# Kernel tuning notes

Hardware: AMD Instinct MI355X
Metric: run time of the kernel (lower is better)

Reference implementation:

```python
import jax, jax.numpy as jnp
import numpy as np
import math

B, L = 4, 2048
D_MODEL, N_HEADS, D_K, D_V, D_FF, FACTOR = 512, 8, 64, 64, 2048, 5


def _layernorm(x, g, b, eps=1e-5):
    m = x.mean(-1, keepdims=True)
    v = jnp.mean((x - m) ** 2, axis=-1, keepdims=True)
    return (x - m) * jax.lax.rsqrt(v + eps) * g + b


def setup_inputs() -> dict:
    key = jax.random.key(0)
    ks = jax.random.split(key, 8)
    w = lambda k, shape: (jax.random.normal(k, shape, jnp.float32) * 0.02)
    sample_k = min(FACTOR * int(math.ceil(math.log(L))), L)  # c*ln(L_K) sampled keys per query
    return {
        "x": jax.random.normal(ks[0], (B, L, D_MODEL), jnp.float32),
        "Wq": w(ks[1], (D_MODEL, N_HEADS * D_K)),
        "Wk": w(ks[2], (D_MODEL, N_HEADS * D_K)),
        "Wv": w(ks[3], (D_MODEL, N_HEADS * D_V)),
        "Wo": w(ks[4], (N_HEADS * D_V, D_MODEL)),
        "ln1_g": jnp.ones((D_MODEL,), jnp.float32),
        "ln1_b": jnp.zeros((D_MODEL,), jnp.float32),
        "conv1_w": w(ks[5], (D_FF, D_MODEL)),
        "conv1_b": jnp.zeros((D_FF,), jnp.float32),
        "conv2_w": w(ks[6], (D_MODEL, D_FF)),
        "conv2_b": jnp.zeros((D_MODEL,), jnp.float32),
        "ln2_g": jnp.ones((D_MODEL,), jnp.float32),
        "ln2_b": jnp.zeros((D_MODEL,), jnp.float32),
        # Informer samples sample_k random keys per query position (constant indices)
        "sample_idx": jax.random.randint(ks[7], (L, sample_k), 0, L),
    }


def reference(x, Wq, Wk, Wv, Wo, ln1_g, ln1_b, conv1_w, conv1_b, conv2_w, conv2_b, ln2_g, ln2_b, sample_idx):
    Bx, Lx, D = x.shape
    H = N_HEADS
    # projections -> [B,H,L,d]
    Q = (x @ Wq).reshape(Bx, Lx, H, D_K).transpose(0, 2, 1, 3)
    K = (x @ Wk).reshape(Bx, Lx, H, D_K).transpose(0, 2, 1, 3)
    V = (x @ Wv).reshape(Bx, Lx, H, D_V).transpose(0, 2, 1, 3)

    u = min(FACTOR * int(math.ceil(math.log(Lx))), Lx)  # top-u active queries
    # sampled QK scores: [B,H,L,sample_k]
    K_samp = K[:, :, sample_idx]                              # [B,H,L,S,dk]
    qk_s = jnp.einsum('bhle,bhlse->bhls', Q, K_samp)
    # sparsity measure M = max - mean (Informer divides sum by L_K)
    M = qk_s.max(-1) - qk_s.sum(-1) / Lx                      # [B,H,L]
    _, top = jax.lax.top_k(M, u)                              # [B,H,u]

    Q_red = jnp.take_along_axis(Q, top[..., None], axis=2)    # [B,H,u,dk]
    scores = jnp.einsum('bhue,bhle->bhul', Q_red, K) / math.sqrt(D_K)
    attn = jax.nn.softmax(scores, axis=-1)                    # [B,H,u,L]

    # initial context = mean of V over keys; update only top-u query rows
    ctx = jnp.broadcast_to(V.mean(axis=2, keepdims=True), V.shape)  # [B,H,L,dv]
    upd = jnp.einsum('bhul,bhld->bhud', attn, V)              # [B,H,u,dv]
    bi = jnp.arange(Bx)[:, None, None]
    hi = jnp.arange(H)[None, :, None]
    ctx = ctx.at[bi, hi, top].set(upd)

    out = ctx.transpose(0, 2, 1, 3).reshape(Bx, Lx, H * D_V) @ Wo
    x1 = _layernorm(x + out, ln1_g, ln1_b)  # residual + norm inside attention sublayer

    # conv1d(k=1) FFN == per-token linear; dropout is identity in eval
    y = jax.nn.gelu(x1 @ conv1_w.T + conv1_b, approximate=False)
    y = y @ conv2_w.T + conv2_b
    return _layernorm(x1 + y, ln2_g, ln2_b)
```

## Files before the change

### kernel.cpp

```cpp
#include <hip/hip_runtime.h>
#include <hip/hip_bf16.h>

#define BB 4
#define LL 2048
#define DD 512
#define HH 8
#define DKK 64
#define FF 2048

typedef __bf16  bf16x8  __attribute__((ext_vector_type(8)));
typedef float   floatx4 __attribute__((ext_vector_type(4)));

__device__ __forceinline__ void async_cp16(const void* g, void* l) {
    __builtin_amdgcn_global_load_lds(
        (const __attribute__((address_space(1))) unsigned int*)g,
        (__attribute__((address_space(3))) unsigned int*)l,
        16, 0, 0);
}

__global__ __launch_bounds__(256) void prep_w(
    const float* __restrict__ Wq, const float* __restrict__ Wk,
    const float* __restrict__ Wv, const float* __restrict__ Wo,
    __bf16* __restrict__ wb)
{
    const size_t SZ = (size_t)DD * DD;
    int z = blockIdx.z;
    const float* s = (z == 0) ? Wq : (z == 1) ? Wk : (z == 2) ? Wv : Wo;
    __bf16* hi; __bf16* lo = nullptr;
    if (z == 0)      { hi = wb;          lo = wb + SZ; }
    else if (z == 1) { hi = wb + 2 * SZ; lo = wb + 3 * SZ; }
    else if (z == 2) { hi = wb + 4 * SZ; }
    else             { hi = wb + 5 * SZ; }
    int idx = blockIdx.x * 256 + threadIdx.x;
    int k = idx >> 9, n = idx & 511;
    float v = s[idx];
    __bf16 h = (__bf16)v;
    hi[(size_t)n * DD + k] = h;
    if (lo) lo[(size_t)n * DD + k] = (__bf16)(v - (float)h);
}

__global__ __launch_bounds__(256) void cast_cw(
    const float* __restrict__ c1w, const float* __restrict__ c2w,
    __bf16* __restrict__ d1, __bf16* __restrict__ d2)
{
    const float* s = blockIdx.z ? c2w : c1w;
    __bf16* d = blockIdx.z ? d2 : d1;
    int idx = blockIdx.x * 256 + threadIdx.x;
    d[idx] = (__bf16)s[idx];
}

__global__ __launch_bounds__(256) void split_cast_x(
    const float* __restrict__ x, __bf16* __restrict__ xhi, __bf16* __restrict__ xlo)
{
    int idx = blockIdx.x * 256 + threadIdx.x;
    float v = x[idx];
    __bf16 h = (__bf16)v;
    xhi[idx] = h;
    xlo[idx] = (__bf16)(v - (float)h);
}

template<int ACT, bool BIAS, bool OUT_BF16>
__global__ __launch_bounds__(256) void gemm_mfma(
    const __bf16* __restrict__ A, const __bf16* __restrict__ B,
    const float* __restrict__ bias, void* __restrict__ Cv,
    int M, int N, int K)
{
    __shared__ __bf16 As[2][128 * 32];
    __shared__ __bf16 Bs[2][128 * 32];
    const int tid = threadIdx.x;
    const int wave = tid >> 6, lane = tid & 63;
    const int gx = gridDim.x;
    const int nwg = gx * gridDim.y;
    const int hw = blockIdx.y * gx + blockIdx.x;
    const int virt = ((nwg & 7) == 0) ? ((hw & 7) * (nwg >> 3) + (hw >> 3)) : hw;
    const int m0 = (virt / gx) * 128, n0 = (virt % gx) * 128;
    const int wm = (wave >> 1) * 64, wn = (wave & 1) * 64;
    const int l15 = lane & 15, kq = lane >> 4;

    auto stage = [&](int buf, int k0) {
        #pragma unroll
        for (int p = 0; p < 2; p++) {
            int c = p * 256 + tid;
            int row = c >> 2, col = (c & 3) * 8;
            async_cp16(A + (size_t)(m0 + row) * K + k0 + col, &As[buf][c * 8]);
            async_cp16(B + (size_t)(n0 + row) * K + k0 + col, &Bs[buf][c * 8]);
        }
    };

    floatx4 acc[4][4] = {};

    stage(0, 0);
    __syncthreads();
    int cur = 0;
    for (int k0 = 0; k0 < K; k0 += 32) {
        if (k0 + 32 < K) stage(cur ^ 1, k0 + 32);
        bf16x8 af[4], bfr[4];
        #pragma unroll
        for (int i = 0; i < 4; i++)
            af[i] = *(const bf16x8*)(&As[cur][(wm + i * 16 + l15) * 32 + kq * 8]);
        #pragma unroll
        for (int j = 0; j < 4; j++)
            bfr[j] = *(const bf16x8*)(&Bs[cur][(wn + j * 16 + l15) * 32 + kq * 8]);
        #pragma unroll
        for (int i = 0; i < 4; i++)
            #pragma unroll
            for (int j = 0; j < 4; j++)
                acc[i][j] = __builtin_amdgcn_mfma_f32_16x16x32_bf16(af[i], bfr[j], acc[i][j], 0, 0, 0);
        __syncthreads();
        cur ^= 1;
    }
    #pragma unroll
    for (int i = 0; i < 4; i++) {
        #pragma unroll
        for (int j = 0; j < 4; j++) {
            int col = n0 + wn + j * 16 + l15;
            float bv = BIAS ? bias[col] : 0.0f;
            #pragma unroll
            for (int r = 0; r < 4; r++) {
                int row = m0 + wm + i * 16 + kq * 4 + r;
                float v = acc[i][j][r] + bv;
                if (ACT == 1) v = 0.5f * v * (1.0f + erff(v * 0.70710678118654752f));
                if (OUT_BF16) ((__bf16*)Cv)[(size_t)row * N + col] = (__bf16)v;
                else          ((float*)Cv)[(size_t)row * N + col] = v;
            }
        }
    }
}

__global__ __launch_bounds__(256) void gemm_mfma_split(
    const __bf16* __restrict__ Ah, const __bf16* __restrict__ Al,
    const __bf16* __restrict__ Bh, const __bf16* __restrict__ Bl,
    float* __restrict__ C, int M, int N, int K)
{
    __shared__ __bf16 Ahs[2][128 * 32];
    __shared__ __bf16 Als[2][128 * 32];
    __shared__ __bf16 Bhs[2][128 * 32];
    __shared__ __bf16 Bls[2][128 * 32];
    const int tid = threadIdx.x;
    const int wave = tid >> 6, lane = tid & 63;
    const int gx = gridDim.x;
    const int nwg = gx * gridDim.y;
    const int hw = blockIdx.y * gx + blockIdx.x;
    const int virt = ((nwg & 7) == 0) ? ((hw & 7) * (nwg >> 3) + (hw >> 3)) : hw;
    const int m0 = (virt / gx) * 128, n0 = (virt % gx) * 128;
    const int wm = (wave >> 1) * 64, wn = (wave & 1) * 64;
    const int l15 = lane & 15, kq = lane >> 4;

    auto stage = [&](int buf, int k0) {
        #pragma unroll
        for (int p = 0; p < 2; p++) {
            int c = p * 256 + tid;
            int row = c >> 2, col = (c & 3) * 8;
            size_t goA = (size_t)(m0 + row) * K + k0 + col;
            size_t goB = (size_t)(n0 + row) * K + k0 + col;
            async_cp16(Ah + goA, &Ahs[buf][c * 8]);
            async_cp16(Al + goA, &Als[buf][c * 8]);
            async_cp16(Bh + goB, &Bhs[buf][c * 8]);
            async_cp16(Bl + goB, &Bls[buf][c * 8]);
        }
    };

    floatx4 acc[4][4] = {};

    stage(0, 0);
    __syncthreads();
    int cur = 0;
    for (int k0 = 0; k0 < K; k0 += 32) {
        if (k0 + 32 < K) stage(cur ^ 1, k0 + 32);
        bf16x8 ah[4], al[4], bh[4], bl[4];
        #pragma unroll
        for (int i = 0; i < 4; i++) {
            int off = (wm + i * 16 + l15) * 32 + kq * 8;
            ah[i] = *(const bf16x8*)(&Ahs[cur][off]);
            al[i] = *(const bf16x8*)(&Als[cur][off]);
        }
        #pragma unroll
        for (int j = 0; j < 4; j++) {
            int off = (wn + j * 16 + l15) * 32 + kq * 8;
            bh[j] = *(const bf16x8*)(&Bhs[cur][off]);
            bl[j] = *(const bf16x8*)(&Bls[cur][off]);
        }
        #pragma unroll
        for (int i = 0; i < 4; i++)
            #pragma unroll
            for (int j = 0; j < 4; j++) {
                acc[i][j] = __builtin_amdgcn_mfma_f32_16x16x32_bf16(ah[i], bh[j], acc[i][j], 0, 0, 0);
                acc[i][j] = __builtin_amdgcn_mfma_f32_16x16x32_bf16(ah[i], bl[j], acc[i][j], 0, 0, 0);
                acc[i][j] = __builtin_amdgcn_mfma_f32_16x16x32_bf16(al[i], bh[j], acc[i][j], 0, 0, 0);
            }
        __syncthreads();
        cur ^= 1;
    }
    #pragma unroll
    for (int i = 0; i < 4; i++)
        #pragma unroll
        for (int j = 0; j < 4; j++) {
            int col = n0 + wn + j * 16 + l15;
            #pragma unroll
            for (int r = 0; r < 4; r++) {
                int row = m0 + wm + i * 16 + kq * 4 + r;
                C[(size_t)row * N + col] = acc[i][j][r];
            }
        }
}

__device__ __forceinline__ float dpp_sum16(float p) {
    int t;
    t = __builtin_amdgcn_update_dpp(0, __float_as_int(p), 0xB1,  0xF, 0xF, true);
    p += __int_as_float(t);
    t = __builtin_amdgcn_update_dpp(0, __float_as_int(p), 0x4E,  0xF, 0xF, true);
    p += __int_as_float(t);
    t = __builtin_amdgcn_update_dpp(0, __float_as_int(p), 0x141, 0xF, 0xF, true);
    p += __int_as_float(t);
    t = __builtin_amdgcn_update_dpp(0, __float_as_int(p), 0x140, 0xF, 0xF, true);
    p += __int_as_float(t);
    return p;
}

__global__ __launch_bounds__(256) void calc_m(
    const float* __restrict__ Q, const float* __restrict__ Kb,
    const int* __restrict__ sidx, float* __restrict__ Mo, int U)
{
    __shared__ int   js[64];
    __shared__ float red_mx[2][HH];
    __shared__ float red_sm[2][HH];
    int i = blockIdx.x;
    int b = i & 3, l = i >> 2;
    int tid = threadIdx.x;
    if (tid < U) js[tid] = sidx[l * U + tid];
    int e    = (tid & 127) * 4;
    int slot = tid >> 7;
    const float* qr = Q + ((size_t)(b * LL + l) * DD);
    float4 q = *(const float4*)(qr + e);
    const float* kbase = Kb + ((size_t)b * LL) * DD + e;
    __syncthreads();
    float mx = -1e30f, sm = 0.f;
    for (int s = slot; s < U; s += 2) {
        int j = js[s];
        float4 kv = *(const float4*)(kbase + (size_t)j * DD);
        float p = q.x * kv.x + q.y * kv.y + q.z * kv.z + q.w * kv.w;
        p = dpp_sum16(p);
        mx = fmaxf(mx, p);
        sm += p;
    }
    if ((tid & 15) == 0) {
        int head = (tid >> 4) & 7;
        red_mx[slot][head] = mx;
        red_sm[slot][head] = sm;
    }
    __syncthreads();
    if (tid < HH) {
        float m2 = fmaxf(red_mx[0][tid], red_mx[1][tid]);
        float s2 = red_sm[0][tid] + red_sm[1][tid];
        Mo[((size_t)(b * HH + tid)) * LL + l] = m2 - s2 * (1.0f / (float)LL);
    }
}

__global__ __launch_bounds__(256) void topk_k(
    const float* __restrict__ Mo, int* __restrict__ top, int U)
{
    __shared__ unsigned int hist[256];
    __shared__ unsigned int wsum[4];
    __shared__ unsigned int bc[2];
    __shared__ int ties[LL];
    __shared__ int cnt2[2];
    int bh = blockIdx.x, tid = threadIdx.x;
    int lane = tid & 63, w = tid >> 6;

    unsigned int my[8];
    #pragma unroll
    for (int i = 0; i < 8; i++) {
        unsigned int u = __float_as_uint(Mo[(size_t)bh * LL + tid + i * 256]);
        my[i] = u ^ ((u >> 31) ? 0xFFFFFFFFu : 0x80000000u);
    }

    unsigned int prefix = 0, pmask = 0;
    unsigned int need = (unsigned int)U;
    unsigned int above = 0;

    for (int pass = 0; pass < 4; pass++) {
        int shift = 24 - pass * 8;
        hist[tid] = 0;
        __syncthreads();
        #pragma unroll
        for (int i = 0; i < 8; i++) {
            unsigned int u = my[i];
            if ((u & pmask) == prefix)
                atomicAdd(&hist[(u >> shift) & 255u], 1u);
        }
        __syncthreads();
        unsigned int h = hist[tid];
        #pragma unroll
        for (int off = 1; off < 64; off <<= 1) {
            unsigned int o = __shfl_down(h, off);
            if (lane + off < 64) h += o;
        }
        if (lane == 0) wsum[w] = h;
        __syncthreads();
        unsigned int tail = 0;
        #pragma unroll
        for (int w2 = 1; w2 < 4; w2++) if (w2 > w) tail += wsum[w2];
        h += tail;
        hist[tid] = h;
        __syncthreads();
        unsigned int St = h;
        unsigned int St1 = (tid < 255) ? hist[tid + 1] : 0u;
        if (St >= need && St1 < need) { bc[0] = (unsigned int)tid; bc[1] = St1; }
        __syncthreads();
        unsigned int dig = bc[0], abv = bc[1];
        above += abv;
        need -= abv;
        prefix |= dig << shift;
        pmask |= 0xFFu << shift;
        __syncthreads();
    }

    if (tid == 0) { cnt2[0] = 0; cnt2[1] = 0; }
    __syncthreads();
    #pragma unroll
    for (int i = 0; i < 8; i++) {
        unsigned int u = my[i];
        int idx = tid + i * 256;
        if (u > prefix) {
            int pos = atomicAdd(&cnt2[0], 1);
            top[bh * U + pos] = idx;
        } else if (u == prefix) {
            int pos = atomicAdd(&cnt2[1], 1);
            ties[pos] = idx;
        }
    }
    __syncthreads();
    int tcnt = cnt2[1];
    #pragma unroll
    for (int i = 0; i < 8; i++) {
        unsigned int u = my[i];
        if (u == prefix) {
            int idx = tid + i * 256;
            int rank = 0;
            for (int j = 0; j < tcnt; j++) rank += (ties[j] < idx) ? 1 : 0;
            if (rank < (int)need) top[bh * U + (int)above + rank] = idx;
        }
    }
}

__global__ __launch_bounds__(256) void vmean_k(
    const __bf16* __restrict__ V, float* __restrict__ Vm)
{
    __shared__ float osum[4][DKK];
    int bh = blockIdx.x;
    int b = bh >> 3, h = bh & 7;
    int tid = threadIdx.x, d = tid & 63, part = tid >> 6;
    const __bf16* vp = V + ((size_t)(b * LL + part * 512) * DD + h * DKK + d);
    float s = 0.f;
    for (int i = 0; i < 512; i++) s += (float)vp[(size_t)i * DD];
    osum[part][d] = s;
    __syncthreads();
    if (tid < DKK)
        Vm[bh * DKK + tid] = (osum[0][tid] + osum[1][tid] + osum[2][tid] + osum[3][tid]) * (1.0f / (float)LL);
}

__global__ __launch_bounds__(256) void gather_qred(
    const float* __restrict__ Q, const int* __restrict__ top,
    __bf16* __restrict__ qred, int U)
{
    int bh = blockIdx.y;
    int b = bh >> 3, h = bh & 7;
    int e = blockIdx.x * 256 + threadIdx.x;
    int u = e >> 6, d = e & 63;
    float v = 0.f;
    if (u < U) {
        int l = top[bh * U + u];
        v = Q[((size_t)(b * LL + l) * DD + h * DKK) + d] * 0.125f;
    }
    qred[(size_t)bh * 48 * DKK + e] = (__bf16)v;
}

__global__ __launch_bounds__(256) void gemm_s(
    const __bf16* __restrict__ qred, const float* __restrict__ Kb,
    float* __restrict__ S)
{
    __shared__ __bf16 Qs[2 * 48 * 32];
    __shared__ __bf16 Ks[2 * 128 * 32];
    int bh = blockIdx.y, nc = blockIdx.x;
    int b = bh >> 3, h = bh & 7, l0 = nc * 128;
    int tid = threadIdx.x;
    const unsigned int* qsrc = (const unsigned int*)(qred + (size_t)bh * 48 * DKK);
    unsigned int* qdst = (unsigned int*)Qs;
    #pragma unroll
    for (int t = 0; t < 6; t++) {
        int ui = tid + t * 256;
        int u = ui >> 5, kp = ui & 31;
        int p = kp >> 4, kl2 = kp & 15;
        qdst[p * 768 + u * 16 + kl2] = qsrc[ui];
    }
    #pragma unroll
    for (int t = 0; t < 8; t++) {
        int fi = tid + t * 256;
        int row = fi >> 4, k4 = fi & 15;
        int p = k4 >> 3, kl = (k4 & 7) * 4;
        float4 kv = *(const float4*)(Kb + ((size_t)(b * LL + l0 + row) * DD + h * DKK + k4 * 4));
        __bf16* dst = Ks + p * 128 * 32 + row * 32 + kl;
        dst[0] = (__bf16)kv.x; dst[1] = (__bf16)kv.y;
        dst[2] = (__bf16)kv.z; dst[3] = (__bf16)kv.w;
    }
    __syncthreads();
    int wave = tid >> 6, lane = tid & 63, l15 = lane & 15, kq = lane >> 4;
    floatx4 acc[3][2] = {};
    #pragma unroll
    for (int p = 0; p < 2; p++) {
        bf16x8 bq[2];
        #pragma unroll
        for (int j = 0; j < 2; j++)
            bq[j] = *(const bf16x8*)(Ks + p * 4096 + (wave * 32 + j * 16 + l15) * 32 + kq * 8);
        #pragma unroll
        for (int i = 0; i < 3; i++) {
            bf16x8 aq = *(const bf16x8*)(Qs + p * 1536 + (i * 16 + l15) * 32 + kq * 8);
            #pragma unroll
            for (int j = 0; j < 2; j++)
                acc[i][j] = __builtin_amdgcn_mfma_f32_16x16x32_bf16(aq, bq[j], acc[i][j], 0, 0, 0);
        }
    }
    #pragma unroll
    for (int i = 0; i < 3; i++)
        #pragma unroll
        for (int j = 0; j < 2; j++) {
            int col = l0 + wave * 32 + j * 16 + l15;
            #pragma unroll
            for (int r = 0; r < 4; r++) {
                int row = i * 16 + kq * 4 + r;
                S[((size_t)bh * 48 + row) * LL + col] = acc[i][j][r];
            }
        }
}

__global__ __launch_bounds__(256) void softmax_p(float* __restrict__ S, int U)
{
    __shared__ float red[256];
    int row = blockIdx.x;
    int bh = row / U, u = row % U;
    float* sr = S + ((size_t)bh * 48 + u) * LL;
    int tid = threadIdx.x;
    float sc[8]; float mx = -1e30f;
    #pragma unroll
    for (int i = 0; i < 8; i++) { sc[i] = sr[tid + i * 256]; mx = fmaxf(mx, sc[i]); }
    red[tid] = mx; __syncthreads();
    for (int s = 128; s > 0; s >>= 1) { if (tid < s) red[tid] = fmaxf(red[tid], red[tid + s]); __syncthreads(); }
    mx = red[0]; __syncthreads();
    float se = 0.f;
    #pragma unroll
    for (int i = 0; i < 8; i++) { sc[i] = __expf(sc[i] - mx); se += sc[i]; }
    red[tid] = se; __syncthreads();
    for (int s = 128; s > 0; s >>= 1) { if (tid < s) red[tid] += red[tid + s]; __syncthreads(); }
    float inv = 1.0f / red[0];
    __bf16* pr = (__bf16*)sr;
    #pragma unroll
    for (int i = 0; i < 8; i++) pr[tid + i * 256] = (__bf16)(sc[i] * inv);
}

__global__ __launch_bounds__(256) void pv_k(
    const float* __restrict__ S, const __bf16* __restrict__ V,
    float* __restrict__ upd, int U)
{
    __shared__ __bf16 pls[4 * LL];
    __shared__ float osum[4][4][DKK];
    int bh = blockIdx.y, uc = blockIdx.x;
    int b = bh >> 3, h = bh & 7, tid = threadIdx.x;
    #pragma unroll
    for (int t = 0; t < 16; t++) {
        int ui = tid + t * 256;
        int up = ui >> 10, lw = ui & 1023;
        const unsigned int* src = (const unsigned int*)(S + ((size_t)bh * 48 + uc * 4 + up) * LL);
        ((unsigned int*)pls)[up * 1024 + lw] = src[lw];
    }
    __syncthreads();
    int d = tid & 63, part = tid >> 6;
    float a0 = 0.f, a1 = 0.f, a2 = 0.f, a3 = 0.f;
    const __bf16* vp = V + ((size_t)(b * LL + part * 512) * DD + h * DKK + d);
    int lbase = part * 512;
    for (int i = 0; i < 512; i++) {
        float v = (float)vp[(size_t)i * DD];
        int l = lbase + i;
        a0 += (float)pls[l] * v;
        a1 += (float)pls[LL + l] * v;
        a2 += (float)pls[2 * LL + l] * v;
        a3 += (float)pls[3 * LL + l] * v;
    }
    osum[part][0][d] = a0; osum[part][1][d] = a1;
    osum[part][2][d] = a2; osum[part][3][d] = a3;
    __syncthreads();
    int u2 = tid >> 6;
    float s = osum[0][u2][d] + osum[1][u2][d] + osum[2][u2][d] + osum[3][u2][d];
    upd[((size_t)bh * U + uc * 4 + u2) * DKK + d] = s;
}

__global__ __launch_bounds__(256) void ctx_init(
    const float* __restrict__ Vm, __bf16* __restrict__ ctx)
{
    int idx = blockIdx.x * 256 + threadIdx.x;
    int c = idx & 511; int h = c >> 6, d = c & 63;
    int bl = idx >> 9; int b = bl >> 11;
    ctx[idx] = (__bf16)Vm[(b * HH + h) * DKK + d];
}
__global__ __launch_bounds__(256) void ctx_scatter(
    const float* __restrict__ upd, const int* __restrict__ top,
    __bf16* __restrict__ ctx, int U, int total)
{
    int idx = blockIdx.x * 256 + threadIdx.x;
    if (idx >= total) return;
    int d = idx & 63; int ru = idx >> 6;
    int bh = ru / U, u = ru % U;
    int b = bh >> 3, h = bh & 7;
    int l = top[bh * U + u];
    ctx[(((size_t)(b * LL + l)) << 9) + h * DKK + d] = (__bf16)upd[idx];
}

__global__ __launch_bounds__(256) void ln1_k(
    const float* __restrict__ x, const float* __restrict__ aout,
    const float* __restrict__ g, const float* __restrict__ bb,
    __bf16* __restrict__ x1h)
{
    __shared__ float red[256];
    int row = blockIdx.x, tid = threadIdx.x;
    size_t base = (size_t)row * DD;
    float h0 = x[base + tid] + aout[base + tid];
    float h1 = x[base + 256 + tid] + aout[base + 256 + tid];
    red[tid] = h0 + h1; __syncthreads();
    for (int s = 128; s > 0; s >>= 1) { if (tid < s) red[tid] += red[tid + s]; __syncthreads(); }
    float mean = red[0] * (1.0f / DD); __syncthreads();
    float d0 = h0 - mean, d1 = h1 - mean;
    red[tid] = d0 * d0 + d1 * d1; __syncthreads();
    for (int s = 128; s > 0; s >>= 1) { if (tid < s) red[tid] += red[tid + s]; __syncthreads(); }
    float rstd = rsqrtf(red[0] * (1.0f / DD) + 1e-5f);
    x1h[base + tid]       = (__bf16)(d0 * rstd * g[tid] + bb[tid]);
    x1h[base + 256 + tid] = (__bf16)(d1 * rstd * g[256 + tid] + bb[256 + tid]);
}

__global__ __launch_bounds__(256) void ln2_k(
    const __bf16* __restrict__ x1h, const float* __restrict__ f2o,
    const float* __restrict__ c2b,
    const float* __restrict__ g, const float* __restrict__ bb,
    float* __restrict__ out)
{
    __shared__ float red[256];
    int row = blockIdx.x, tid = threadIdx.x;
    size_t base = (size_t)row * DD;
    float h0 = (float)x1h[base + tid] + f2o[base + tid] + c2b[tid];
    float h1 = (float)x1h[base + 256 + tid] + f2o[base + 256 + tid] + c2b[256 + tid];
    red[tid] = h0 + h1; __syncthreads();
    for (int s = 128; s > 0; s >>= 1) { if (tid < s) red[tid] += red[tid + s]; __syncthreads(); }
    float mean = red[0] * (1.0f / DD); __syncthreads();
    float d0 = h0 - mean, d1 = h1 - mean;
    red[tid] = d0 * d0 + d1 * d1; __syncthreads();
    for (int s = 128; s > 0; s >>= 1) { if (tid < s) red[tid] += red[tid + s]; __syncthreads(); }
    float rstd = rsqrtf(red[0] * (1.0f / DD) + 1e-5f);
    out[base + tid]       = d0 * rstd * g[tid] + bb[tid];
    out[base + 256 + tid] = d1 * rstd * g[256 + tid] + bb[256 + tid];
}

extern "C" void kernel_launch(void* const* d_in, const int* in_sizes, int n_in,
                              void* d_out, int out_size, void* d_ws, size_t ws_size,
                              hipStream_t stream)
{
    const float* x   = (const float*)d_in[0];
    const float* Wq  = (const float*)d_in[1];
    const float* Wk  = (const float*)d_in[2];
    const float* Wv  = (const float*)d_in[3];
    const float* Wo  = (const float*)d_in[4];
    const float* g1  = (const float*)d_in[5];
    const float* b1  = (const float*)d_in[6];
    const float* c1w = (const float*)d_in[7];
    const float* c1b = (const float*)d_in[8];
    const float* c2w = (const float*)d_in[9];
    const float* c2b = (const float*)d_in[10];
    const float* g2  = (const float*)d_in[11];
    const float* b2  = (const float*)d_in[12];
    const int* sidx  = (const int*)d_in[13];
    float* out       = (float*)d_out;

    const int U = in_sizes[13] / LL;
    const int M = BB * LL;

    char* ws = (char*)d_ws;
    const size_t MB = (size_t)1 << 20;
    float*  Q    = (float*)(ws + 0);
    float*  Kb   = (float*)(ws + 16 * MB);
    __bf16* V    = (__bf16*)(ws + 32 * MB);
    __bf16* xhi  = (__bf16*)(ws + 40 * MB);
    __bf16* xlo  = (__bf16*)(ws + 48 * MB);
    float*  S    = (float*)(ws + 40 * MB);
    __bf16* wb   = (__bf16*)(ws + 56 * MB);
    __bf16* c1wb = (__bf16*)(ws + 59 * MB);
    __bf16* c2wb = (__bf16*)(ws + 61 * MB);
    float*  Mo   = (float*)(ws + 63 * MB);
    float*  upd  = (float*)(ws + 63 * MB + 256 * 1024);
    float*  Vm   = (float*)(ws + 63 * MB + 576 * 1024);
    int*    top  = (int*)  (ws + 63 * MB + 584 * 1024);
    __bf16* qred = (__bf16*)(ws + 63 * MB + 592 * 1024);
    float*  aout = Q;
    float*  f2o  = Q;
    __bf16* ctx  = V;
    __bf16* ych  = (__bf16*)(ws + 16 * MB);
    __bf16* x1h  = xlo;
    (void)ws_size; (void)n_in; (void)out_size;

    const size_t SZ = (size_t)DD * DD;
    __bf16* WqThi = wb;          __bf16* WqTlo = wb + SZ;
    __bf16* WkThi = wb + 2 * SZ; __bf16* WkTlo = wb + 3 * SZ;
    __bf16* WvT   = wb + 4 * SZ; __bf16* WoT   = wb + 5 * SZ;

    prep_w<<<dim3(DD * DD / 256, 1, 4), 256, 0, stream>>>(Wq, Wk, Wv, Wo, wb);
    cast_cw<<<dim3(FF * DD / 256, 1, 2), 256, 0, stream>>>(c1w, c2w, c1wb, c2wb);
    split_cast_x<<<BB * LL * DD / 256, 256, 0, stream>>>(x, xhi, xlo);

    dim3 gproj(DD / 128, M / 128);
    gemm_mfma_split<<<gproj, 256, 0, stream>>>(xhi, xlo, WqThi, WqTlo, Q,  M, DD, DD);
    gemm_mfma_split<<<gproj, 256, 0, stream>>>(xhi, xlo, WkThi, WkTlo, Kb, M, DD, DD);
    gemm_mfma<0, false, true ><<<gproj, 256, 0, stream>>>(xhi, WvT, nullptr, V, M, DD, DD);

    calc_m<<<BB * LL, 256, 0, stream>>>(Q, Kb, sidx, Mo, U);
    topk_k<<<BB * HH, 256, 0, stream>>>(Mo, top, U);
    vmean_k<<<BB * HH, 256, 0, stream>>>(V, Vm);

    gather_qred<<<dim3(48 * DKK / 256, BB * HH), 256, 0, stream>>>(Q, top, qred, U);
    gemm_s<<<dim3(LL / 128, BB * HH), 256, 0, stream>>>(qred, Kb, S);
    softmax_p<<<BB * HH * U, 256, 0, stream>>>(S, U);
    pv_k<<<dim3(U / 4, BB * HH), 256, 0, stream>>>(S, V, upd, U);

    ctx_init<<<M * DD / 256, 256, 0, stream>>>(Vm, ctx);
    int sc_total = BB * HH * U * DKK;
    ctx_scatter<<<(sc_total + 255) / 256, 256, 0, stream>>>(upd, top, ctx, U, sc_total);
    gemm_mfma<0, false, false><<<gproj, 256, 0, stream>>>(ctx, WoT, nullptr, aout, M, DD, DD);

    ln1_k<<<M, 256, 0, stream>>>(x, aout, g1, b1, x1h);

    gemm_mfma<1, true,  true ><<<dim3(FF / 128, M / 128), 256, 0, stream>>>(x1h, c1wb, c1b, ych, M, FF, DD);
    gemm_mfma<0, false, false><<<dim3(DD / 128, M / 128), 256, 0, stream>>>(ych, c2wb, nullptr, f2o, M, DD, FF);

    ln2_k<<<M, 256, 0, stream>>>(x1h, f2o, c2b, g2, b2, out);
}
```

Baseline: 420.5 us.

## Swizzle GEMM LDS tiles and stage epilogue through LDS for vector stores

XOR-swizzles the 16-byte chunk position in the LDS A/B tiles of both GEMM kernels so the MFMA fragment reads hit fewer bank conflicts. It also rewrites the epilogues to write accumulators into a padded LDS buffer (unioned with the staging tiles) and then emit row-contiguous 16-byte global stores, replacing the scattered scalar stores. This adds extra barriers and an LDS round-trip at the end of each tile, and the fp32 path needs two passes because of LDS capacity.

New measurement: 472.0 us. +12.2%, slower.

```diff
diff --git a/kernel.cpp b/kernel.cpp
--- a/kernel.cpp
+++ b/kernel.cpp
@@ -65,8 +65,12 @@
     const float* __restrict__ bias, void* __restrict__ Cv,
     int M, int N, int K)
 {
-    __shared__ __bf16 As[2][128 * 32];
-    __shared__ __bf16 Bs[2][128 * 32];
+    union SmemT {
+        struct { __bf16 A[2][128 * 32]; __bf16 B[2][128 * 32]; } st;
+        __bf16 ebf[128 * 136];
+        float  ef[64 * 132];
+    };
+    __shared__ SmemT sm;
     const int tid = threadIdx.x;
     const int wave = tid >> 6, lane = tid & 63;
     const int gx = gridDim.x;
@@ -81,9 +85,10 @@
         #pragma unroll
         for (int p = 0; p < 2; p++) {
             int c = p * 256 + tid;
-            int row = c >> 2, col = (c & 3) * 8;
-            async_cp16(A + (size_t)(m0 + row) * K + k0 + col, &As[buf][c * 8]);
-            async_cp16(B + (size_t)(n0 + row) * K + k0 + col, &Bs[buf][c * 8]);
+            int row = c >> 2;
+            int col = ((c & 3) ^ ((row >> 1) & 3)) * 8;
+            async_cp16(A + (size_t)(m0 + row) * K + k0 + col, &sm.st.A[buf][c * 8]);
+            async_cp16(B + (size_t)(n0 + row) * K + k0 + col, &sm.st.B[buf][c * 8]);
         }
     };
 
@@ -96,11 +101,15 @@
         if (k0 + 32 < K) stage(cur ^ 1, k0 + 32);
         bf16x8 af[4], bfr[4];
         #pragma unroll
-        for (int i = 0; i < 4; i++)
-            af[i] = *(const bf16x8*)(&As[cur][(wm + i * 16 + l15) * 32 + kq * 8]);
-        #pragma unroll
-        for (int j = 0; j < 4; j++)
-            bfr[j] = *(const bf16x8*)(&Bs[cur][(wn + j * 16 + l15) * 32 + kq * 8]);
+        for (int i = 0; i < 4; i++) {
+            int ra = wm + i * 16 + l15;
+            af[i] = *(const bf16x8*)(&sm.st.A[cur][ra * 32 + ((kq ^ ((ra >> 1) & 3)) << 3)]);
+        }
+        #pragma unroll
+        for (int j = 0; j < 4; j++) {
+            int rb = wn + j * 16 + l15;
+            bfr[j] = *(const bf16x8*)(&sm.st.B[cur][rb * 32 + ((kq ^ ((rb >> 1) & 3)) << 3)]);
+        }
         #pragma unroll
         for (int i = 0; i < 4; i++)
             #pragma unroll
@@ -109,19 +118,56 @@
         __syncthreads();
         cur ^= 1;
     }
-    #pragma unroll
-    for (int i = 0; i < 4; i++) {
-        #pragma unroll
-        for (int j = 0; j < 4; j++) {
-            int col = n0 + wn + j * 16 + l15;
-            float bv = BIAS ? bias[col] : 0.0f;
+
+    if (OUT_BF16) {
+        #pragma unroll
+        for (int i = 0; i < 4; i++)
             #pragma unroll
-            for (int r = 0; r < 4; r++) {
-                int row = m0 + wm + i * 16 + kq * 4 + r;
-                float v = acc[i][j][r] + bv;
-                if (ACT == 1) v = 0.5f * v * (1.0f + erff(v * 0.70710678118654752f));
-                if (OUT_BF16) ((__bf16*)Cv)[(size_t)row * N + col] = (__bf16)v;
-                else          ((float*)Cv)[(size_t)row * N + col] = v;
+            for (int j = 0; j < 4; j++) {
+                int col = wn + j * 16 + l15;
+                float bv = BIAS ? bias[n0 + col] : 0.0f;
+                #pragma unroll
+                for (int r = 0; r < 4; r++) {
+                    int row = wm + i * 16 + kq * 4 + r;
+                    float v = acc[i][j][r] + bv;
+                    if (ACT == 1) v = 0.5f * v * (1.0f + erff(v * 0.70710678118654752f));
+                    sm.ebf[row * 136 + col] = (__bf16)v;
+                }
+            }
+        __syncthreads();
+        #pragma unroll
+        for (int t = 0; t < 8; t++) {
+            int rr = (wave << 5) + (t << 2) + kq;
+            float4 vv = *(const float4*)&sm.ebf[rr * 136 + l15 * 8];
+            *(float4*)((__bf16*)Cv + (size_t)(m0 + rr) * N + n0 + l15 * 8) = vv;
+        }
+    } else {
+        const int l31 = lane & 31, hi = lane >> 5;
+        #pragma unroll
+        for (int pass = 0; pass < 2; pass++) {
+            __syncthreads();
+            if ((wave >> 1) == pass) {
+                #pragma unroll
+                for (int i = 0; i < 4; i++)
+                    #pragma unroll
+                    for (int j = 0; j < 4; j++) {
+                        int col = wn + j * 16 + l15;
+                        float bv = BIAS ? bias[n0 + col] : 0.0f;
+                        #pragma unroll
+                        for (int r = 0; r < 4; r++) {
+                            int rl = i * 16 + kq * 4 + r;
+                            float v = acc[i][j][r] + bv;
+                            if (ACT == 1) v = 0.5f * v * (1.0f + erff(v * 0.70710678118654752f));
+                            sm.ef[rl * 132 + col] = v;
+                        }
+                    }
+            }
+            __syncthreads();
+            #pragma unroll
+            for (int t = 0; t < 8; t++) {
+                int rl = t * 8 + wave * 2 + hi;
+                float4 vv = *(const float4*)&sm.ef[rl * 132 + l31 * 4];
+                *(float4*)((float*)Cv + (size_t)(m0 + pass * 64 + rl) * N + n0 + l31 * 4) = vv;
             }
         }
     }
@@ -132,10 +178,12 @@
     const __bf16* __restrict__ Bh, const __bf16* __restrict__ Bl,
     float* __restrict__ C, int M, int N, int K)
 {
-    __shared__ __bf16 Ahs[2][128 * 32];
-    __shared__ __bf16 Als[2][128 * 32];
-    __shared__ __bf16 Bhs[2][128 * 32];
-    __shared__ __bf16 Bls[2][128 * 32];
+    union SmemS {
+        struct { __bf16 Ah[2][128 * 32]; __bf16 Al[2][128 * 32];
+                 __bf16 Bh[2][128 * 32]; __bf16 Bl[2][128 * 32]; } st;
+        float ef[64 * 132];
+    };
+    __shared__ SmemS sm;
     const int tid = threadIdx.x;
     const int wave = tid >> 6, lane = tid & 63;
     const int gx = gridDim.x;
@@ -150,13 +198,14 @@
         #pragma unroll
         for (int p = 0; p < 2; p++) {
             int c = p * 256 + tid;
-            int row = c >> 2, col = (c & 3) * 8;
+            int row = c >> 2;
+            int col = ((c & 3) ^ ((row >> 1) & 3)) * 8;
             size_t goA = (size_t)(m0 + row) * K + k0 + col;
             size_t goB = (size_t)(n0 + row) * K + k0 + col;
-            async_cp16(Ah + goA, &Ahs[buf][c * 8]);
-            async_cp16(Al + goA, &Als[buf][c * 8]);
-            async_cp16(Bh + goB, &Bhs[buf][c * 8]);
-            async_cp16(Bl + goB, &Bls[buf][c * 8]);
+            async_cp16(Ah + goA, &sm.st.Ah[buf][c * 8]);
+            async_cp16(Al + goA, &sm.st.Al[buf][c * 8]);
+            async_cp16(Bh + goB, &sm.st.Bh[buf][c * 8]);
+            async_cp16(Bl + goB, &sm.st.Bl[buf][c * 8]);
         }
     };
 
@@ -170,15 +219,17 @@
         bf16x8 ah[4], al[4], bh[4], bl[4];
         #pragma unroll
         for (int i = 0; i < 4; i++) {
-            int off = (wm + i * 16 + l15) * 32 + kq * 8;
-            ah[i] = *(const bf16x8*)(&Ahs[cur][off]);
-            al[i] = *(const bf16x8*)(&Als[cur][off]);
+            int ra = wm + i * 16 + l15;
+            int off = ra * 32 + ((kq ^ ((ra >> 1) & 3)) << 3);
+            ah[i] = *(const bf16x8*)(&sm.st.Ah[cur][off]);
+            al[i] = *(const bf16x8*)(&sm.st.Al[cur][off]);
         }
         #pragma unroll
         for (int j = 0; j < 4; j++) {
-            int off = (wn + j * 16 + l15) * 32 + kq * 8;
-            bh[j] = *(const bf16x8*)(&Bhs[cur][off]);
-            bl[j] = *(const bf16x8*)(&Bls[cur][off]);
+            int rb = wn + j * 16 + l15;
+            int off = rb * 32 + ((kq ^ ((rb >> 1) & 3)) << 3);
+            bh[j] = *(const bf16x8*)(&sm.st.Bh[cur][off]);
+            bl[j] = *(const bf16x8*)(&sm.st.Bl[cur][off]);
         }
         #pragma unroll
         for (int i = 0; i < 4; i++)
@@ -191,17 +242,32 @@
         __syncthreads();
         cur ^= 1;
     }
-    #pragma unroll
-    for (int i = 0; i < 4; i++)
-        #pragma unroll
-        for (int j = 0; j < 4; j++) {
-            int col = n0 + wn + j * 16 + l15;
+
+    const int l31 = lane & 31, hi = lane >> 5;
+    #pragma unroll
+    for (int pass = 0; pass < 2; pass++) {
+        __syncthreads();
+        if ((wave >> 1) == pass) {
             #pragma unroll
-            for (int r = 0; r < 4; r++) {
-                int row = m0 + wm + i * 16 + kq * 4 + r;
-                C[(size_t)row * N + col] = acc[i][j][r];
-            }
-        }
+            for (int i = 0; i < 4; i++)
+                #pragma unroll
+                for (int j = 0; j < 4; j++) {
+                    int col = wn + j * 16 + l15;
+                    #pragma unroll
+                    for (int r = 0; r < 4; r++) {
+                        int rl = i * 16 + kq * 4 + r;
+                        sm.ef[rl * 132 + col] = acc[i][j][r];
+                    }
+                }
+        }
+        __syncthreads();
+        #pragma unroll
+        for (int t = 0; t < 8; t++) {
+            int rl = t * 8 + wave * 2 + hi;
+            float4 vv = *(const float4*)&sm.ef[rl * 132 + l31 * 4];
+            *(float4*)(C + (size_t)(m0 + pass * 64 + rl) * N + n0 + l31 * 4) = vv;
+        }
+    }
 }
 
 __device__ __forceinline__ float dpp_sum16(float p) {
```
